# Performance work log

Hardware: AMD Instinct MI355X
Metric: run time of the kernel (lower is better)

The kernel has to match this reference:

```python
import jax, jax.numpy as jnp
import numpy as np

DIM = 1024
HEADS = 16
HEAD_DIM = 64
INNER = HEADS * HEAD_DIM  # 1024
EPS = 1e-5


def setup_inputs() -> dict:
    key = jax.random.key(0)
    ks = jax.random.split(key, 6)
    b, s = 4, 2048
    x = jax.random.normal(ks[0], (b, s, DIM), dtype=jnp.float32)
    # LayerNorm params
    ln_g = jnp.ones((DIM,), dtype=jnp.float32)
    ln_b = jnp.zeros((DIM,), dtype=jnp.float32)
    # qkv projection (torch Linear: y = x @ W.T + b); store as [DIM, 3*INNER] for x @ W
    w_qkv = jax.random.normal(ks[1], (DIM, 3 * INNER), dtype=jnp.float32) / np.sqrt(DIM)
    b_qkv = jax.random.normal(ks[2], (3 * INNER,), dtype=jnp.float32) * 0.01
    w_out = jax.random.normal(ks[3], (INNER, DIM), dtype=jnp.float32) / np.sqrt(INNER)
    b_out = jax.random.normal(ks[4], (DIM,), dtype=jnp.float32) * 0.01
    return {"x": x, "ln_g": ln_g, "ln_b": ln_b, "w_qkv": w_qkv,
            "b_qkv": b_qkv, "w_out": w_out, "b_out": b_out}


def reference(x, ln_g, ln_b, w_qkv, b_qkv, w_out, b_out):
    b, s, _ = x.shape
    scale = HEAD_DIM ** -0.5
    # Pre-norm LayerNorm over last dim
    mu = jnp.mean(x, axis=-1, keepdims=True)
    var = jnp.mean(jnp.square(x - mu), axis=-1, keepdims=True)
    xn = (x - mu) * jax.lax.rsqrt(var + EPS) * ln_g + ln_b
    # QKV projection, split into q,k,v (chunk along last dim)
    qkv = xn @ w_qkv + b_qkv  # [b, s, 3*INNER]
    q, k, v = jnp.split(qkv, 3, axis=-1)
    # [b, s, INNER] -> [b, heads, s, head_dim]
    def split_heads(t):
        return t.reshape(b, s, HEADS, HEAD_DIM).transpose(0, 2, 1, 3)
    q, k, v = split_heads(q), split_heads(k), split_heads(v)
    scores = jnp.einsum('bnqd,bnkd->bnqk', q, k) * scale  # [b, h, s, s]
    probs = jax.nn.softmax(scores, axis=-1)  # dropout p=0.0 (eval)
    out = jnp.einsum('bnqk,bnkd->bnqd', probs, v)  # [b, h, s, d]
    out = out.transpose(0, 2, 1, 3).reshape(b, s, INNER)
    return out @ w_out + b_out
```

## Files before the change

### kernel.cpp

```cpp
#include <hip/hip_runtime.h>
#include <hip/hip_bf16.h>

#define DIM 1024
#define HEADS 16
#define HEAD_DIM 64
#define INNER 1024
#define SEQ 2048
#define BATCH 4
#define ROWS (BATCH * SEQ)
#define QKV_N (3 * INNER)

using short4v = __attribute__((ext_vector_type(4))) short;
using short8 = __attribute__((ext_vector_type(8))) short;
using f32x4  = __attribute__((ext_vector_type(4))) float;

#define BM 128
#define BN 128
#define BK 64
#define LDT 72
#define ALD 68

#define CSC 0.18033688011112042f

__global__ __launch_bounds__(256)
void transpose_cast_kernel(const float* __restrict__ in,
                           __hip_bfloat16* __restrict__ outp, int R, int C)
{
    __shared__ __align__(16) __hip_bfloat16 tile[64][LDT];
    const int t  = threadIdx.x;
    const int r0 = blockIdx.y * 64, c0 = blockIdx.x * 64;
    const int ltr = t >> 4, ltc = (t & 15) * 4;
    #pragma unroll
    for (int p = 0; p < 4; ++p) {
        int rr = ltr + p * 16;
        float4 v = *(const float4*)(in + (size_t)(r0 + rr) * C + c0 + ltc);
        tile[rr][ltc + 0] = __float2bfloat16(v.x);
        tile[rr][ltc + 1] = __float2bfloat16(v.y);
        tile[rr][ltc + 2] = __float2bfloat16(v.z);
        tile[rr][ltc + 3] = __float2bfloat16(v.w);
    }
    __syncthreads();
    const int wtr = t >> 3, wtc = (t & 7) * 8;
    #pragma unroll
    for (int p = 0; p < 2; ++p) {
        int oc = wtr + p * 32;
        union { uint4 v; __hip_bfloat16 h[8]; } u;
        #pragma unroll
        for (int j = 0; j < 8; ++j) u.h[j] = tile[wtc + j][oc];
        *(uint4*)(outp + (size_t)(c0 + oc) * R + r0 + wtc) = u.v;
    }
}

__global__ __launch_bounds__(256)
void v_transpose_kernel(const __hip_bfloat16* __restrict__ qkv,
                        __hip_bfloat16* __restrict__ vT)
{
    __shared__ __align__(16) __hip_bfloat16 tile[64][LDT];
    const int t  = threadIdx.x;
    const int st = blockIdx.x;
    const int bh = blockIdx.y, b = bh >> 4, h = bh & 15;
    const __hip_bfloat16* src =
        qkv + (size_t)(b * SEQ + st * 64) * QKV_N + 2 * INNER + h * HEAD_DIM;
    const int lr = t >> 3, lc = (t & 7) * 8;
    #pragma unroll
    for (int p = 0; p < 2; ++p) {
        int r = lr + p * 32;
        *(uint4*)&tile[r][lc] = *(const uint4*)(src + (size_t)r * QKV_N + lc);
    }
    __syncthreads();
    __hip_bfloat16* dst = vT + (size_t)bh * HEAD_DIM * SEQ + st * 64;
    #pragma unroll
    for (int p = 0; p < 2; ++p) {
        int d = lr + p * 32;
        union { uint4 v; __hip_bfloat16 h8[8]; } u;
        #pragma unroll
        for (int j = 0; j < 8; ++j) u.h8[j] = tile[lc + j][d];
        *(uint4*)(dst + (size_t)d * SEQ + lc) = u.v;
    }
}

__global__ __launch_bounds__(256)
void ln_kernel(const float* __restrict__ x,
               const float* __restrict__ g,
               const float* __restrict__ b,
               __hip_bfloat16* __restrict__ y)
{
    const int wave = threadIdx.x >> 6;
    const int lane = threadIdx.x & 63;
    const int row  = blockIdx.x * 4 + wave;
    const float* xr = x + (size_t)row * DIM + lane * 16;

    float xs[16];
    #pragma unroll
    for (int q = 0; q < 4; ++q) {
        float4 v = *(const float4*)(xr + q * 4);
        xs[q * 4 + 0] = v.x; xs[q * 4 + 1] = v.y;
        xs[q * 4 + 2] = v.z; xs[q * 4 + 3] = v.w;
    }
    float sum = 0.f, sq = 0.f;
    #pragma unroll
    for (int i = 0; i < 16; ++i) { sum += xs[i]; sq += xs[i] * xs[i]; }
    #pragma unroll
    for (int off = 32; off; off >>= 1) {
        sum += __shfl_xor(sum, off);
        sq  += __shfl_xor(sq,  off);
    }
    const float mu  = sum * (1.0f / DIM);
    const float var = sq * (1.0f / DIM) - mu * mu;
    const float rs  = rsqrtf(var + 1e-5f);

    const float* gp = g + lane * 16;
    const float* bp = b + lane * 16;
    union { uint4 v[2]; __hip_bfloat16 h[16]; } yu;
    #pragma unroll
    for (int q = 0; q < 4; ++q) {
        float4 gv = *(const float4*)(gp + q * 4);
        float4 bv = *(const float4*)(bp + q * 4);
        yu.h[q * 4 + 0] = __float2bfloat16((xs[q * 4 + 0] - mu) * rs * gv.x + bv.x);
        yu.h[q * 4 + 1] = __float2bfloat16((xs[q * 4 + 1] - mu) * rs * gv.y + bv.y);
        yu.h[q * 4 + 2] = __float2bfloat16((xs[q * 4 + 2] - mu) * rs * gv.z + bv.z);
        yu.h[q * 4 + 3] = __float2bfloat16((xs[q * 4 + 3] - mu) * rs * gv.w + bv.w);
    }
    __hip_bfloat16* yr = y + (size_t)row * DIM + lane * 16;
    *(uint4*)yr       = yu.v[0];
    *(uint4*)(yr + 8) = yu.v[1];
}

__device__ inline void store_out(__hip_bfloat16* p, float v) { *p = __float2bfloat16(v); }
__device__ inline void store_out(float* p, float v)          { *p = v; }

template <bool QSCALE, typename OutT>
__global__ __launch_bounds__(256)
void gemm_bt_bias(const __hip_bfloat16* __restrict__ A,
                  const __hip_bfloat16* __restrict__ Bt,
                  const float* __restrict__ bias,
                  OutT* __restrict__ C,
                  int M, int N, int K)
{
    __shared__ __align__(16) __hip_bfloat16 As[BM * BK];
    __shared__ __align__(16) __hip_bfloat16 Bs[BN * BK];

    const int t    = threadIdx.x;
    const int wave = t >> 6,  lane = t & 63;
    const int wm   = wave >> 1, wn = wave & 1;
    const int quad = lane >> 4, l16 = lane & 15;
    const int m0   = blockIdx.y * BM, n0 = blockIdx.x * BN;
    const int sr   = t >> 3, scol = (t & 7) * 8;

    f32x4 acc[4][4];
    #pragma unroll
    for (int i = 0; i < 4; ++i)
        #pragma unroll
        for (int j = 0; j < 4; ++j)
            acc[i][j] = (f32x4){0.f, 0.f, 0.f, 0.f};

    const __hip_bfloat16* Ab = A  + (size_t)(m0 + sr) * K + scol;
    const __hip_bfloat16* Bb = Bt + (size_t)(n0 + sr) * K + scol;

    for (int k0 = 0; k0 < K; k0 += BK) {
        __syncthreads();
        #pragma unroll
        for (int p = 0; p < 4; ++p) {
            __builtin_amdgcn_global_load_lds(
                (const __attribute__((address_space(1))) void*)(Ab + (size_t)(p * 32) * K + k0),
                (__attribute__((address_space(3))) void*)(&As[(sr + p * 32) * BK + scol]),
                16, 0, 0);
            __builtin_amdgcn_global_load_lds(
                (const __attribute__((address_space(1))) void*)(Bb + (size_t)(p * 32) * K + k0),
                (__attribute__((address_space(3))) void*)(&Bs[(sr + p * 32) * BK + scol]),
                16, 0, 0);
        }
        __syncthreads();
        #pragma unroll
        for (int kk = 0; kk < BK; kk += 32) {
            short8 af[4], bfr[4];
            const int ac = kk + quad * 8;
            #pragma unroll
            for (int mt = 0; mt < 4; ++mt)
                af[mt] = *(const short8*)&As[(wm * 64 + mt * 16 + l16) * BK + ac];
            #pragma unroll
            for (int nt = 0; nt < 4; ++nt)
                bfr[nt] = *(const short8*)&Bs[(wn * 64 + nt * 16 + l16) * BK + ac];
            #pragma unroll
            for (int mt = 0; mt < 4; ++mt)
                #pragma unroll
                for (int nt = 0; nt < 4; ++nt)
                    acc[mt][nt] = __builtin_amdgcn_mfma_f32_16x16x32_bf16(
                        af[mt], bfr[nt], acc[mt][nt], 0, 0, 0);
        }
    }

    #pragma unroll
    for (int nt = 0; nt < 4; ++nt) {
        const int col = n0 + wn * 64 + nt * 16 + l16;
        const float bv = bias[col];
        const float scale = (QSCALE && col < INNER) ? CSC : 1.0f;
        #pragma unroll
        for (int mt = 0; mt < 4; ++mt) {
            const int rowb = m0 + wm * 64 + mt * 16 + quad * 4;
            #pragma unroll
            for (int r = 0; r < 4; ++r)
                store_out(&C[(size_t)(rowb + r) * N + col], (acc[mt][nt][r] + bv) * scale);
        }
    }
}

__global__ __launch_bounds__(256)
void attn_kernel(const __hip_bfloat16* __restrict__ qkv,
                 const __hip_bfloat16* __restrict__ vT,
                 __hip_bfloat16* __restrict__ outp)
{
    __shared__ __align__(16) __hip_bfloat16 smem[128 * ALD];
    __hip_bfloat16* Ks = smem;
    __hip_bfloat16* Vt = smem + 64 * ALD;

    const int t    = threadIdx.x;
    const int wave = t >> 6, lane = t & 63;
    const int quad = lane >> 4, l16 = lane & 15;
    const int bh   = blockIdx.y, batch = bh >> 4, head = bh & 15;
    const int q0   = blockIdx.x * 128;
    const __hip_bfloat16* qbase = qkv + (size_t)batch * SEQ * QKV_N + head * HEAD_DIM;
    const __hip_bfloat16* kbase = qbase + INNER;
    const __hip_bfloat16* vbase = vT + (size_t)bh * HEAD_DIM * SEQ;
    const int lr = t >> 3, lc = (t & 7) * 8;

    short8 qf[2][2];
    #pragma unroll
    for (int nt = 0; nt < 2; ++nt)
        #pragma unroll
        for (int kk = 0; kk < 2; ++kk)
            qf[nt][kk] = *(const short8*)(qbase
                + (size_t)(q0 + wave * 32 + nt * 16 + l16) * QKV_N + kk * 32 + quad * 8);

    float l_acc[2] = {0.f, 0.f};
    f32x4 o_acc[2][4];
    #pragma unroll
    for (int nt = 0; nt < 2; ++nt)
        #pragma unroll
        for (int dt = 0; dt < 4; ++dt) o_acc[nt][dt] = (f32x4){0.f, 0.f, 0.f, 0.f};

    for (int kv0 = 0; kv0 < SEQ; kv0 += 64) {
        __syncthreads();
        #pragma unroll
        for (int p = 0; p < 2; ++p) {
            int r = lr + p * 32;
            *(uint4*)&Ks[r * ALD + lc] =
                *(const uint4*)(kbase + (size_t)(kv0 + r) * QKV_N + lc);
            *(uint4*)&Vt[r * ALD + lc] =
                *(const uint4*)(vbase + (size_t)r * SEQ + kv0 + lc);
        }
        __syncthreads();

        #pragma unroll
        for (int mt = 0; mt < 4; ++mt) {
            f32x4 sc[2];
            sc[0] = (f32x4){0.f, 0.f, 0.f, 0.f};
            sc[1] = (f32x4){0.f, 0.f, 0.f, 0.f};
            #pragma unroll
            for (int kk = 0; kk < 2; ++kk) {
                short8 a = *(const short8*)&Ks[(mt * 16 + l16) * ALD + kk * 32 + quad * 8];
                #pragma unroll
                for (int nt = 0; nt < 2; ++nt)
                    sc[nt] = __builtin_amdgcn_mfma_f32_16x16x32_bf16(a, qf[nt][kk], sc[nt], 0, 0, 0);
            }
            short4v pf[2];
            #pragma unroll
            for (int nt = 0; nt < 2; ++nt) {
                union { short4v s4; __hip_bfloat16 h[4]; } u;
                #pragma unroll
                for (int r = 0; r < 4; ++r) {
                    float p = exp2f(sc[nt][r]);
                    l_acc[nt] += p;
                    u.h[r] = __float2bfloat16(p);
                }
                pf[nt] = u.s4;
            }
            #pragma unroll
            for (int dt = 0; dt < 4; ++dt) {
                short4v a = *(const short4v*)&Vt[(dt * 16 + l16) * ALD + mt * 16 + quad * 4];
                #pragma unroll
                for (int nt = 0; nt < 2; ++nt)
                    o_acc[nt][dt] = __builtin_amdgcn_mfma_f32_16x16x16bf16_1k(
                        a, pf[nt], o_acc[nt][dt], 0, 0, 0);
            }
        }
    }

    float inv[2];
    #pragma unroll
    for (int nt = 0; nt < 2; ++nt) {
        float l = l_acc[nt];
        l += __shfl_xor(l, 16);
        l += __shfl_xor(l, 32);
        inv[nt] = 1.0f / l;
    }

    __syncthreads();
    #pragma unroll
    for (int nt = 0; nt < 2; ++nt)
        #pragma unroll
        for (int dt = 0; dt < 4; ++dt) {
            union { short4v s4; __hip_bfloat16 h[4]; } u;
            #pragma unroll
            for (int r = 0; r < 4; ++r)
                u.h[r] = __float2bfloat16(o_acc[nt][dt][r] * inv[nt]);
            *(short4v*)&smem[(wave * 32 + nt * 16 + l16) * ALD + dt * 16 + quad * 4] = u.s4;
        }
    __syncthreads();
    #pragma unroll
    for (int p = 0; p < 4; ++p) {
        int r = lr + p * 32;
        uint4 v = *(const uint4*)&smem[r * ALD + lc];
        *(uint4*)(outp + (size_t)(batch * SEQ + q0 + r) * INNER
                  + head * HEAD_DIM + lc) = v;
    }
}

extern "C" void kernel_launch(void* const* d_in, const int* in_sizes, int n_in,
                              void* d_out, int out_size, void* d_ws, size_t ws_size,
                              hipStream_t stream)
{
    const float* x    = (const float*)d_in[0];
    const float* ln_g = (const float*)d_in[1];
    const float* ln_b = (const float*)d_in[2];
    const float* wqkv = (const float*)d_in[3];
    const float* bqkv = (const float*)d_in[4];
    const float* wout = (const float*)d_in[5];
    const float* bout = (const float*)d_in[6];
    float* out = (float*)d_out;

    __hip_bfloat16* xn    = (__hip_bfloat16*)d_ws;
    __hip_bfloat16* qkv   = xn    + (size_t)ROWS * DIM;
    __hip_bfloat16* vTbuf = qkv   + (size_t)ROWS * QKV_N;
    __hip_bfloat16* wqkvT = vTbuf + (size_t)BATCH * HEADS * HEAD_DIM * SEQ;
    __hip_bfloat16* woutT = wqkvT + (size_t)QKV_N * DIM;
    __hip_bfloat16* attno = xn;

    transpose_cast_kernel<<<dim3(QKV_N / 64, DIM / 64), 256, 0, stream>>>(wqkv, wqkvT, DIM, QKV_N);
    transpose_cast_kernel<<<dim3(DIM / 64, INNER / 64), 256, 0, stream>>>(wout, woutT, INNER, DIM);
    ln_kernel<<<ROWS / 4, 256, 0, stream>>>(x, ln_g, ln_b, xn);
    gemm_bt_bias<true, __hip_bfloat16><<<dim3(QKV_N / BN, ROWS / BM), 256, 0, stream>>>(
        xn, wqkvT, bqkv, qkv, ROWS, QKV_N, DIM);
    v_transpose_kernel<<<dim3(SEQ / 64, BATCH * HEADS), 256, 0, stream>>>(qkv, vTbuf);
    attn_kernel<<<dim3(SEQ / 128, BATCH * HEADS), 256, 0, stream>>>(qkv, vTbuf, attno);
    gemm_bt_bias<false, float><<<dim3(DIM / BN, ROWS / BM), 256, 0, stream>>>(
        attno, woutT, bout, out, ROWS, DIM, INNER);
}
```

Measured before the change: 397.7 us.

## Permute V transpose layout so attention loads V fragments with wide LDS reads

The V transpose kernel now writes keys in a permuted order so that each lane's four 16-key MFMA fragments are contiguous, letting the attention loop load them with two 16-byte LDS reads per d-tile instead of four 8-byte reads. The attention loop is restructured to compute all QK^T scores for the 64-key block first, then exponentiate, then run PV MFMAs, which gives the scheduler more independent work. It also switches to the hardware exp2 builtin and packed bf16x2 conversions. The cost is more registers live at once (all scores and probabilities for the block) and a layout coupling between the two kernels.

Measured after the change: 552.1 us. +38.8%, slower.

```diff
diff --git a/kernel.cpp b/kernel.cpp
--- a/kernel.cpp
+++ b/kernel.cpp
@@ -69,12 +69,17 @@
     }
     __syncthreads();
     __hip_bfloat16* dst = vT + (size_t)bh * HEAD_DIM * SEQ + st * 64;
+    const int qd = lc >> 4;
     #pragma unroll
     for (int p = 0; p < 2; ++p) {
         int d = lr + p * 32;
         union { uint4 v; __hip_bfloat16 h8[8]; } u;
         #pragma unroll
-        for (int j = 0; j < 8; ++j) u.h8[j] = tile[lc + j][d];
+        for (int j8 = 0; j8 < 8; ++j8) {
+            int pp = lc + j8;
+            int kv = 16 * ((pp >> 2) & 3) + 4 * qd + (pp & 3);
+            u.h8[j8] = tile[kv][d];
+        }
         *(uint4*)(dst + (size_t)d * SEQ + lc) = u.v;
     }
 }
@@ -226,18 +231,18 @@
 
     short8 qf[2][2];
     #pragma unroll
-    for (int nt = 0; nt < 2; ++nt)
+    for (int nq = 0; nq < 2; ++nq)
         #pragma unroll
         for (int kk = 0; kk < 2; ++kk)
-            qf[nt][kk] = *(const short8*)(qbase
-                + (size_t)(q0 + wave * 32 + nt * 16 + l16) * QKV_N + kk * 32 + quad * 8);
+            qf[nq][kk] = *(const short8*)(qbase
+                + (size_t)(q0 + wave * 32 + nq * 16 + l16) * QKV_N + kk * 32 + quad * 8);
 
     float l_acc[2] = {0.f, 0.f};
     f32x4 o_acc[2][4];
     #pragma unroll
-    for (int nt = 0; nt < 2; ++nt)
-        #pragma unroll
-        for (int dt = 0; dt < 4; ++dt) o_acc[nt][dt] = (f32x4){0.f, 0.f, 0.f, 0.f};
+    for (int nq = 0; nq < 2; ++nq)
+        #pragma unroll
+        for (int dt = 0; dt < 4; ++dt) o_acc[nq][dt] = (f32x4){0.f, 0.f, 0.f, 0.f};
 
     for (int kv0 = 0; kv0 < SEQ; kv0 += 64) {
         __syncthreads();
@@ -251,60 +256,81 @@
         }
         __syncthreads();
 
-        #pragma unroll
-        for (int mt = 0; mt < 4; ++mt) {
-            f32x4 sc[2];
-            sc[0] = (f32x4){0.f, 0.f, 0.f, 0.f};
-            sc[1] = (f32x4){0.f, 0.f, 0.f, 0.f};
+        f32x4 sc[2][4];
+        #pragma unroll
+        for (int nq = 0; nq < 2; ++nq)
+            #pragma unroll
+            for (int mt = 0; mt < 4; ++mt) sc[nq][mt] = (f32x4){0.f, 0.f, 0.f, 0.f};
+        #pragma unroll
+        for (int mt = 0; mt < 4; ++mt)
             #pragma unroll
             for (int kk = 0; kk < 2; ++kk) {
                 short8 a = *(const short8*)&Ks[(mt * 16 + l16) * ALD + kk * 32 + quad * 8];
                 #pragma unroll
-                for (int nt = 0; nt < 2; ++nt)
-                    sc[nt] = __builtin_amdgcn_mfma_f32_16x16x32_bf16(a, qf[nt][kk], sc[nt], 0, 0, 0);
+                for (int nq = 0; nq < 2; ++nq)
+                    sc[nq][mt] = __builtin_amdgcn_mfma_f32_16x16x32_bf16(
+                        a, qf[nq][kk], sc[nq][mt], 0, 0, 0);
             }
-            short4v pf[2];
-            #pragma unroll
-            for (int nt = 0; nt < 2; ++nt) {
-                union { short4v s4; __hip_bfloat16 h[4]; } u;
-                #pragma unroll
-                for (int r = 0; r < 4; ++r) {
-                    float p = exp2f(sc[nt][r]);
-                    l_acc[nt] += p;
-                    u.h[r] = __float2bfloat16(p);
-                }
-                pf[nt] = u.s4;
+
+        short4v pf[2][4];
+        #pragma unroll
+        for (int nq = 0; nq < 2; ++nq)
+            #pragma unroll
+            for (int mt = 0; mt < 4; ++mt) {
+                float p0 = __builtin_amdgcn_exp2f(sc[nq][mt][0]);
+                float p1 = __builtin_amdgcn_exp2f(sc[nq][mt][1]);
+                float p2 = __builtin_amdgcn_exp2f(sc[nq][mt][2]);
+                float p3 = __builtin_amdgcn_exp2f(sc[nq][mt][3]);
+                l_acc[nq] += (p0 + p1) + (p2 + p3);
+                union { short4v s4; __hip_bfloat162 b2[2]; } u;
+                u.b2[0] = __float22bfloat162_rn(make_float2(p0, p1));
+                u.b2[1] = __float22bfloat162_rn(make_float2(p2, p3));
+                pf[nq][mt] = u.s4;
             }
-            #pragma unroll
-            for (int dt = 0; dt < 4; ++dt) {
-                short4v a = *(const short4v*)&Vt[(dt * 16 + l16) * ALD + mt * 16 + quad * 4];
-                #pragma unroll
-                for (int nt = 0; nt < 2; ++nt)
-                    o_acc[nt][dt] = __builtin_amdgcn_mfma_f32_16x16x16bf16_1k(
-                        a, pf[nt], o_acc[nt][dt], 0, 0, 0);
+
+        #pragma unroll
+        for (int dt = 0; dt < 4; ++dt) {
+            const __hip_bfloat16* vr = &Vt[(dt * 16 + l16) * ALD + 16 * quad];
+            short8 v0 = *(const short8*)vr;
+            short8 v1 = *(const short8*)(vr + 8);
+            short4v a0 = __builtin_shufflevector(v0, v0, 0, 1, 2, 3);
+            short4v a1 = __builtin_shufflevector(v0, v0, 4, 5, 6, 7);
+            short4v a2 = __builtin_shufflevector(v1, v1, 0, 1, 2, 3);
+            short4v a3 = __builtin_shufflevector(v1, v1, 4, 5, 6, 7);
+            #pragma unroll
+            for (int nq = 0; nq < 2; ++nq) {
+                o_acc[nq][dt] = __builtin_amdgcn_mfma_f32_16x16x16bf16_1k(
+                    a0, pf[nq][0], o_acc[nq][dt], 0, 0, 0);
+                o_acc[nq][dt] = __builtin_amdgcn_mfma_f32_16x16x16bf16_1k(
+                    a1, pf[nq][1], o_acc[nq][dt], 0, 0, 0);
+                o_acc[nq][dt] = __builtin_amdgcn_mfma_f32_16x16x16bf16_1k(
+                    a2, pf[nq][2], o_acc[nq][dt], 0, 0, 0);
+                o_acc[nq][dt] = __builtin_amdgcn_mfma_f32_16x16x16bf16_1k(
+                    a3, pf[nq][3], o_acc[nq][dt], 0, 0, 0);
             }
         }
     }
 
     float inv[2];
     #pragma unroll
-    for (int nt = 0; nt < 2; ++nt) {
-        float l = l_acc[nt];
+    for (int nq = 0; nq < 2; ++nq) {
+        float l = l_acc[nq];
         l += __shfl_xor(l, 16);
         l += __shfl_xor(l, 32);
-        inv[nt] = 1.0f / l;
+        inv[nq] = 1.0f / l;
     }
 
     __syncthreads();
     #pragma unroll
-    for (int nt = 0; nt < 2; ++nt)
+    for (int nq = 0; nq < 2; ++nq)
         #pragma unroll
         for (int dt = 0; dt < 4; ++dt) {
-            union { short4v s4; __hip_bfloat16 h[4]; } u;
-            #pragma unroll
-            for (int r = 0; r < 4; ++r)
-                u.h[r] = __float2bfloat16(o_acc[nt][dt][r] * inv[nt]);
-            *(short4v*)&smem[(wave * 32 + nt * 16 + l16) * ALD + dt * 16 + quad * 4] = u.s4;
+            union { short4v s4; __hip_bfloat162 b2[2]; } u;
+            u.b2[0] = __float22bfloat162_rn(
+                make_float2(o_acc[nq][dt][0] * inv[nq], o_acc[nq][dt][1] * inv[nq]));
+            u.b2[1] = __float22bfloat162_rn(
+                make_float2(o_acc[nq][dt][2] * inv[nq], o_acc[nq][dt][3] * inv[nq]));
+            *(short4v*)&smem[(wave * 32 + nq * 16 + l16) * ALD + dt * 16 + quad * 4] = u.s4;
         }
     __syncthreads();
     #pragma unroll
```
